# Optimization experiments

Hardware: AMD Instinct MI355X
Metric: run time of the kernel (lower is better)

Reference implementation:

```python
import jax, jax.numpy as jnp
import numpy as np

BATCH = 1024
INPUT_DIM = 4096
HIDDEN_DIM = 4096
N_BLOCKS = 8
BLOCK_SIZE = HIDDEN_DIM // N_BLOCKS          # 512
IN_BLOCK_SIZE = INPUT_DIM // N_BLOCKS        # 512


def setup_inputs() -> dict:
    key = jax.random.key(0)
    ks = jax.random.split(key, 6)
    scale = 1.0 / np.sqrt(BLOCK_SIZE)  # torch GRUCell init: U(-1/sqrt(hidden), 1/sqrt(hidden))
    return {
        "x": jax.random.normal(ks[0], (BATCH, INPUT_DIM), dtype=jnp.float32),
        "h": jax.random.normal(ks[1], (BATCH, HIDDEN_DIM), dtype=jnp.float32),
        "W_ih": jax.random.normal(ks[2], (N_BLOCKS, 3 * BLOCK_SIZE, IN_BLOCK_SIZE), dtype=jnp.float32) * scale,
        "W_hh": jax.random.normal(ks[3], (N_BLOCKS, 3 * BLOCK_SIZE, BLOCK_SIZE), dtype=jnp.float32) * scale,
        "b_ih": jax.random.normal(ks[4], (N_BLOCKS, 3 * BLOCK_SIZE), dtype=jnp.float32) * scale,
        "b_hh": jax.random.normal(ks[5], (N_BLOCKS, 3 * BLOCK_SIZE), dtype=jnp.float32) * scale,
    }


def reference(x, h, W_ih, W_hh, b_ih, b_hh):
    B = x.shape[0]
    n, g3, ibs = W_ih.shape           # n_blocks, 3*block_size, input_block_size
    bs = W_hh.shape[2]                # block_size
    xb = x.reshape(B, n, ibs)         # (B, n_blocks, input_block_size)
    hb = h.reshape(B, n, bs)          # (B, n_blocks, block_size)
    # Block-diagonal GEMM: one grouped matmul over all blocks at once.
    gi = jnp.einsum('bni,ngi->bng', xb, W_ih) + b_ih   # (B, n, 3*bs)
    gh = jnp.einsum('bnh,ngh->bng', hb, W_hh) + b_hh   # (B, n, 3*bs)
    i_r, i_z, i_n = jnp.split(gi, 3, axis=-1)
    h_r, h_z, h_n = jnp.split(gh, 3, axis=-1)
    r = jax.nn.sigmoid(i_r + h_r)                      # reset gate
    z = jax.nn.sigmoid(i_z + h_z)                      # update gate
    n_gate = jnp.tanh(i_n + r * h_n)                   # candidate state
    new_h = n_gate + z * (hb - n_gate)                 # torch GRUCell: h' = (1-z)*n + z*h
    return new_h.reshape(B, n * bs)
```

## Files before the change

### kernel.cpp

```cpp
#include <hip/hip_runtime.h>
#include <hip/hip_bf16.h>
#include <stdint.h>

#define G1CAST(p) ((const __attribute__((address_space(1))) void*)(p))
#define L3CAST(p) ((__attribute__((address_space(3))) void*)(p))

typedef short bf16x8 __attribute__((ext_vector_type(8)));
typedef float f32x16 __attribute__((ext_vector_type(16)));

static __device__ __forceinline__ short f2bf(float f) {
    __hip_bfloat16 b = __float2bfloat16(f);
    return __builtin_bit_cast(short, b);
}

__global__ __launch_bounds__(256) void wconv_kernel(const float* __restrict__ Wih,
                                                    const float* __restrict__ Whh,
                                                    short* __restrict__ Wcat) {
    const int tid = blockIdx.x * 256 + threadIdx.x;
    const int64_t e = (int64_t)tid * 8;
    const int kk = (int)(e & 1023);
    const int row = (int)(e >> 10);
    const int n = row / 1536;
    const int gr = row - n * 1536;
    const float* src = (kk < 512)
        ? Wih + ((int64_t)n * 786432 + (int64_t)gr * 512 + kk)
        : Whh + ((int64_t)n * 786432 + (int64_t)gr * 512 + (kk - 512));
    const float4 a = ((const float4*)src)[0];
    const float4 b = ((const float4*)src)[1];
    bf16x8 o;
    o[0] = f2bf(a.x); o[1] = f2bf(a.y); o[2] = f2bf(a.z); o[3] = f2bf(a.w);
    o[4] = f2bf(b.x); o[5] = f2bf(b.y); o[6] = f2bf(b.z); o[7] = f2bf(b.w);
    *(bf16x8*)(Wcat + e) = o;
}

__global__ __launch_bounds__(256) void aconv_kernel(const float* __restrict__ x,
                                                    const float* __restrict__ h,
                                                    short* __restrict__ Aimg) {
    const int gid = blockIdx.x * 256 + threadIdx.x;
    const int q = gid & 511;
    const int tile = gid >> 9;
    const int c4 = q & 3;
    const int r = q >> 2;
    const int ks = tile & 31;
    const int nblk = (tile >> 5) & 7;
    const int bt = tile >> 8;
    const float* base = (ks < 16) ? x : h;
    const float* src = base + ((size_t)(bt * 128 + r) * 4096
                               + nblk * 512 + (ks & 15) * 32 + c4 * 8);
    const float4 a = ((const float4*)src)[0];
    const float4 b = ((const float4*)src)[1];
    bf16x8 o;
    o[0] = f2bf(a.x); o[1] = f2bf(a.y); o[2] = f2bf(a.z); o[3] = f2bf(a.w);
    o[4] = f2bf(b.x); o[5] = f2bf(b.y); o[6] = f2bf(b.z); o[7] = f2bf(b.w);
    *(bf16x8*)(Aimg + (size_t)tile * 4096 + r * 32 + ((c4 ^ ((r >> 1) & 3)) * 8)) = o;
}

__global__ __launch_bounds__(512, 4) void gru_kernel(
    const float* __restrict__ hst,
    const short* __restrict__ Wcat, const short* __restrict__ Aimg,
    const float* __restrict__ b_ih, const float* __restrict__ b_hh,
    float* __restrict__ out)
{
    __shared__ short ldsA[4][128 * 32];
    __shared__ short ldsB[4][3 * 64 * 32];

    const int tid = threadIdx.x;
    const int nblk = blockIdx.x & 7;
    const int rr_ = blockIdx.x >> 3;
    const int bt = rr_ >> 3;
    const int jt = rr_ & 7;
    const int j0b = jt * 64;
    const int brow0 = bt * 128;

    const int lane = tid & 63;
    const int wave = tid >> 6;
    const int wm = wave >> 1;
    const int wn = wave & 1;
    const int l31 = lane & 31;
    const int k8 = lane >> 5;

    const int bj  = (tid & 255) >> 2;
    const int cir = tid & 3;
    const int g1  = tid >> 8;
    const size_t bsrc1 = ((size_t)nblk * 1536 + (size_t)g1 * 512 + (size_t)(j0b + bj)) * 1024
                       + (size_t)((cir ^ ((bj >> 1) & 3)) * 8);
    const size_t bsrc2 = bsrc1 + (size_t)2 * 512 * 1024;
    const size_t a_tile0 = ((size_t)(bt * 8 + nblk) * 32) << 13;

    f32x16 acc_r = {};
    f32x16 acc_z = {};
    f32x16 acc_nx = {};
    f32x16 acc_nh = {};

    auto stage = [&](int buf, int ks) {
        const char* asrc = (const char*)Aimg + a_tile0 + ((size_t)ks << 13) + (size_t)tid * 16;
        __builtin_amdgcn_global_load_lds(G1CAST(asrc),
                                         L3CAST((char*)&ldsA[buf][0] + tid * 16), 16, 0, 0);
        const short* ws = Wcat + (size_t)ks * 32;
        __builtin_amdgcn_global_load_lds(G1CAST(ws + bsrc1),
                                         L3CAST((char*)&ldsB[buf][0] + tid * 16), 16, 0, 0);
        if (tid < 256)
            __builtin_amdgcn_global_load_lds(G1CAST(ws + bsrc2),
                                             L3CAST((char*)&ldsB[buf][0] + 8192 + tid * 16), 16, 0, 0);
    };

    const int arow = wm * 32 + l31;
    const int aoff = arow * 64;
    const int aswz = ((arow >> 1) & 3) << 4;
    const int jl = wn * 32 + l31;
    const int boff = jl * 64;
    const int bswz = ((jl >> 1) & 3) << 4;

    auto computeStep = [&](const short* Ab_s, const short* Bb_s, f32x16& accN) {
        const char* Ab = (const char*)Ab_s;
        const char* Bb = (const char*)Bb_s;
        #pragma unroll
        for (int ksub = 0; ksub < 2; ++ksub) {
            const int kb = ksub * 32 + k8 * 16;
            bf16x8 af = *(const bf16x8*)(Ab + aoff + (kb ^ aswz));
            bf16x8 b0 = *(const bf16x8*)(Bb + 0 * 4096 + boff + (kb ^ bswz));
            bf16x8 b1 = *(const bf16x8*)(Bb + 1 * 4096 + boff + (kb ^ bswz));
            bf16x8 b2 = *(const bf16x8*)(Bb + 2 * 4096 + boff + (kb ^ bswz));
            acc_r = __builtin_amdgcn_mfma_f32_32x32x16_bf16(af, b0, acc_r, 0, 0, 0);
            acc_z = __builtin_amdgcn_mfma_f32_32x32x16_bf16(af, b1, acc_z, 0, 0, 0);
            accN  = __builtin_amdgcn_mfma_f32_32x32x16_bf16(af, b2, accN, 0, 0, 0);
        }
    };

    stage(0, 0); stage(1, 1); stage(2, 2);

    #pragma unroll 1
    for (int i = 0; i < 16; ++i) {
        asm volatile("s_waitcnt vmcnt(4)" ::: "memory");
        __builtin_amdgcn_s_barrier();
        stage((i + 3) & 3, i + 3);
        computeStep(ldsA[i & 3], ldsB[i & 3], acc_nx);
    }
    #pragma unroll 1
    for (int i = 16; i < 29; ++i) {
        asm volatile("s_waitcnt vmcnt(4)" ::: "memory");
        __builtin_amdgcn_s_barrier();
        stage((i + 3) & 3, i + 3);
        computeStep(ldsA[i & 3], ldsB[i & 3], acc_nh);
    }
    asm volatile("s_waitcnt vmcnt(4)" ::: "memory");
    __builtin_amdgcn_s_barrier();
    computeStep(ldsA[29 & 3], ldsB[29 & 3], acc_nh);
    asm volatile("s_waitcnt vmcnt(2)" ::: "memory");
    __builtin_amdgcn_s_barrier();
    computeStep(ldsA[30 & 3], ldsB[30 & 3], acc_nh);
    asm volatile("s_waitcnt vmcnt(0)" ::: "memory");
    __builtin_amdgcn_s_barrier();
    computeStep(ldsA[31 & 3], ldsB[31 & 3], acc_nh);

    const int jb = j0b + wn * 32 + l31;
    const int bb = nblk * 1536 + jb;
    const float br = b_ih[bb] + b_hh[bb];
    const float bz = b_ih[bb + 512] + b_hh[bb + 512];
    const float bnx = b_ih[bb + 1024];
    const float bnh = b_hh[bb + 1024];
    const int gcol = nblk * 512 + jb;
    #pragma unroll
    for (int rr = 0; rr < 16; ++rr) {
        const int rowl = (rr & 3) + 8 * (rr >> 2) + 4 * k8;
        const int row = brow0 + wm * 32 + rowl;
        const size_t idx = (size_t)row * 4096 + gcol;
        const float sr = acc_r[rr] + br;
        const float sz = acc_z[rr] + bz;
        const float rg = 1.f / (1.f + __expf(-sr));
        const float zg = 1.f / (1.f + __expf(-sz));
        const float tin = (acc_nx[rr] + bnx) + rg * (acc_nh[rr] + bnh);
        const float e2 = __expf(-2.f * tin);
        const float ng = 2.f / (1.f + e2) - 1.f;
        const float hv = hst[idx];
        out[idx] = ng + zg * (hv - ng);
    }
}

extern "C" void kernel_launch(void* const* d_in, const int* in_sizes, int n_in,
                              void* d_out, int out_size, void* d_ws, size_t ws_size,
                              hipStream_t stream) {
    (void)in_sizes; (void)n_in; (void)out_size; (void)ws_size;
    const float* x    = (const float*)d_in[0];
    const float* h    = (const float*)d_in[1];
    const float* W_ih = (const float*)d_in[2];
    const float* W_hh = (const float*)d_in[3];
    const float* b_ih = (const float*)d_in[4];
    const float* b_hh = (const float*)d_in[5];
    short* Wcat = (short*)d_ws;
    short* Aimg = (short*)d_ws + (size_t)12 * 1024 * 1024;

    wconv_kernel<<<6144, 256, 0, stream>>>(W_ih, W_hh, Wcat);
    aconv_kernel<<<4096, 256, 0, stream>>>(x, h, Aimg);
    gru_kernel<<<512, 512, 0, stream>>>(h, Wcat, Aimg, b_ih, b_hh, (float*)d_out);
}
```

Before: 61.02 us.

## Double batch tile to 256 rows so each block reuses weights across two M sub-tiles

Each workgroup now covers 256 batch rows instead of 128, with each wave computing two 32-row MFMA sub-tiles that share the same B fragments. The A-image layout and staging loads change to match, the grid halves to 256 blocks, and launch bounds drop to 2 blocks per CU. This halves weight traffic per output but doubles accumulator registers and leaves only one block per CU, which reduces latency hiding.

```diff
diff --git a/kernel.cpp b/kernel.cpp
--- a/kernel.cpp
+++ b/kernel.cpp
@@ -37,32 +37,31 @@
                                                     const float* __restrict__ h,
                                                     short* __restrict__ Aimg) {
     const int gid = blockIdx.x * 256 + threadIdx.x;
-    const int q = gid & 511;
-    const int tile = gid >> 9;
-    const int c4 = q & 3;
-    const int r = q >> 2;
+    const int c4 = gid & 3;
+    const int r = (gid >> 2) & 255;
+    const int tile = gid >> 10;
     const int ks = tile & 31;
     const int nblk = (tile >> 5) & 7;
     const int bt = tile >> 8;
     const float* base = (ks < 16) ? x : h;
-    const float* src = base + ((size_t)(bt * 128 + r) * 4096
+    const float* src = base + ((size_t)(bt * 256 + r) * 4096
                                + nblk * 512 + (ks & 15) * 32 + c4 * 8);
     const float4 a = ((const float4*)src)[0];
     const float4 b = ((const float4*)src)[1];
     bf16x8 o;
     o[0] = f2bf(a.x); o[1] = f2bf(a.y); o[2] = f2bf(a.z); o[3] = f2bf(a.w);
     o[4] = f2bf(b.x); o[5] = f2bf(b.y); o[6] = f2bf(b.z); o[7] = f2bf(b.w);
-    *(bf16x8*)(Aimg + (size_t)tile * 4096 + r * 32 + ((c4 ^ ((r >> 1) & 3)) * 8)) = o;
-}
-
-__global__ __launch_bounds__(512, 4) void gru_kernel(
+    *(bf16x8*)(Aimg + (size_t)tile * 8192 + r * 32 + ((c4 ^ ((r >> 1) & 3)) * 8)) = o;
+}
+
+__global__ __launch_bounds__(512, 2) void gru_kernel(
     const float* __restrict__ hst,
     const short* __restrict__ Wcat, const short* __restrict__ Aimg,
     const float* __restrict__ b_ih, const float* __restrict__ b_hh,
     float* __restrict__ out)
 {
-    __shared__ short ldsA[4][128 * 32];
-    __shared__ short ldsB[4][3 * 64 * 32];
+    __shared__ short ldsA[4][8192];
+    __shared__ short ldsB[4][8192];
 
     const int tid = threadIdx.x;
     const int nblk = blockIdx.x & 7;
@@ -70,7 +69,7 @@
     const int bt = rr_ >> 3;
     const int jt = rr_ & 7;
     const int j0b = jt * 64;
-    const int brow0 = bt * 128;
+    const int brow0 = bt * 256;
 
     const int lane = tid & 63;
     const int wave = tid >> 6;
@@ -79,51 +78,58 @@
     const int l31 = lane & 31;
     const int k8 = lane >> 5;
 
-    const int bj  = (tid & 255) >> 2;
-    const int cir = tid & 3;
-    const int g1  = tid >> 8;
-    const size_t bsrc1 = ((size_t)nblk * 1536 + (size_t)g1 * 512 + (size_t)(j0b + bj)) * 1024
-                       + (size_t)((cir ^ ((bj >> 1) & 3)) * 8);
-    const size_t bsrc2 = bsrc1 + (size_t)2 * 512 * 1024;
-    const size_t a_tile0 = ((size_t)(bt * 8 + nblk) * 32) << 13;
-
-    f32x16 acc_r = {};
-    f32x16 acc_z = {};
-    f32x16 acc_nx = {};
-    f32x16 acc_nh = {};
+    auto bsrc_of = [&](int c) -> size_t {
+        const int g = c >> 8, j = (c & 255) >> 2, ci = c & 3;
+        return ((size_t)nblk * 1536 + (size_t)g * 512 + (size_t)(j0b + j)) * 1024
+             + (size_t)((ci ^ ((j >> 1) & 3)) * 8);
+    };
+    const size_t bsrc0 = bsrc_of(tid);
+    const size_t bsrc1 = bsrc_of(tid < 256 ? tid + 512 : tid + 256);
+    const size_t a_tile0 = ((size_t)(bt * 8 + nblk) * 32) << 14;
+
+    f32x16 acc_r[2] = {};
+    f32x16 acc_z[2] = {};
+    f32x16 acc_nx[2] = {};
+    f32x16 acc_nh[2] = {};
 
     auto stage = [&](int buf, int ks) {
-        const char* asrc = (const char*)Aimg + a_tile0 + ((size_t)ks << 13) + (size_t)tid * 16;
-        __builtin_amdgcn_global_load_lds(G1CAST(asrc),
-                                         L3CAST((char*)&ldsA[buf][0] + tid * 16), 16, 0, 0);
+        const char* asrc = (const char*)Aimg + a_tile0 + ((size_t)ks << 14) + (size_t)tid * 16;
+        char* adst = (char*)&ldsA[buf][0] + tid * 16;
+        __builtin_amdgcn_global_load_lds(G1CAST(asrc), L3CAST(adst), 16, 0, 0);
+        __builtin_amdgcn_global_load_lds(G1CAST(asrc + 8192), L3CAST(adst + 8192), 16, 0, 0);
         const short* ws = Wcat + (size_t)ks * 32;
-        __builtin_amdgcn_global_load_lds(G1CAST(ws + bsrc1),
-                                         L3CAST((char*)&ldsB[buf][0] + tid * 16), 16, 0, 0);
-        if (tid < 256)
-            __builtin_amdgcn_global_load_lds(G1CAST(ws + bsrc2),
-                                             L3CAST((char*)&ldsB[buf][0] + 8192 + tid * 16), 16, 0, 0);
+        char* bdst = (char*)&ldsB[buf][0] + tid * 16;
+        __builtin_amdgcn_global_load_lds(G1CAST(ws + bsrc0), L3CAST(bdst), 16, 0, 0);
+        __builtin_amdgcn_global_load_lds(G1CAST(ws + bsrc1), L3CAST(bdst + 8192), 16, 0, 0);
     };
 
-    const int arow = wm * 32 + l31;
-    const int aoff = arow * 64;
-    const int aswz = ((arow >> 1) & 3) << 4;
     const int jl = wn * 32 + l31;
     const int boff = jl * 64;
     const int bswz = ((jl >> 1) & 3) << 4;
-
-    auto computeStep = [&](const short* Ab_s, const short* Bb_s, f32x16& accN) {
+    const int arow0 = wm * 64 + l31;
+    const int arow1 = arow0 + 32;
+    const int aoff0 = arow0 * 64;
+    const int aoff1 = arow1 * 64;
+    const int aswz0 = ((arow0 >> 1) & 3) << 4;
+    const int aswz1 = ((arow1 >> 1) & 3) << 4;
+
+    auto computeStep = [&](const short* Ab_s, const short* Bb_s, f32x16 (&accN)[2]) {
         const char* Ab = (const char*)Ab_s;
         const char* Bb = (const char*)Bb_s;
         #pragma unroll
         for (int ksub = 0; ksub < 2; ++ksub) {
             const int kb = ksub * 32 + k8 * 16;
-            bf16x8 af = *(const bf16x8*)(Ab + aoff + (kb ^ aswz));
+            bf16x8 af0 = *(const bf16x8*)(Ab + aoff0 + (kb ^ aswz0));
+            bf16x8 af1 = *(const bf16x8*)(Ab + aoff1 + (kb ^ aswz1));
             bf16x8 b0 = *(const bf16x8*)(Bb + 0 * 4096 + boff + (kb ^ bswz));
             bf16x8 b1 = *(const bf16x8*)(Bb + 1 * 4096 + boff + (kb ^ bswz));
             bf16x8 b2 = *(const bf16x8*)(Bb + 2 * 4096 + boff + (kb ^ bswz));
-            acc_r = __builtin_amdgcn_mfma_f32_32x32x16_bf16(af, b0, acc_r, 0, 0, 0);
-            acc_z = __builtin_amdgcn_mfma_f32_32x32x16_bf16(af, b1, acc_z, 0, 0, 0);
-            accN  = __builtin_amdgcn_mfma_f32_32x32x16_bf16(af, b2, accN, 0, 0, 0);
+            acc_r[0] = __builtin_amdgcn_mfma_f32_32x32x16_bf16(af0, b0, acc_r[0], 0, 0, 0);
+            acc_r[1] = __builtin_amdgcn_mfma_f32_32x32x16_bf16(af1, b0, acc_r[1], 0, 0, 0);
+            acc_z[0] = __builtin_amdgcn_mfma_f32_32x32x16_bf16(af0, b1, acc_z[0], 0, 0, 0);
+            acc_z[1] = __builtin_amdgcn_mfma_f32_32x32x16_bf16(af1, b1, acc_z[1], 0, 0, 0);
+            accN[0]  = __builtin_amdgcn_mfma_f32_32x32x16_bf16(af0, b2, accN[0], 0, 0, 0);
+            accN[1]  = __builtin_amdgcn_mfma_f32_32x32x16_bf16(af1, b2, accN[1], 0, 0, 0);
         }
     };
 
@@ -131,25 +137,30 @@
 
     #pragma unroll 1
     for (int i = 0; i < 16; ++i) {
-        asm volatile("s_waitcnt vmcnt(4)" ::: "memory");
+        asm volatile("s_waitcnt vmcnt(8)" ::: "memory");
+        __builtin_amdgcn_sched_barrier(0);
         __builtin_amdgcn_s_barrier();
         stage((i + 3) & 3, i + 3);
         computeStep(ldsA[i & 3], ldsB[i & 3], acc_nx);
     }
     #pragma unroll 1
     for (int i = 16; i < 29; ++i) {
-        asm volatile("s_waitcnt vmcnt(4)" ::: "memory");
+        asm volatile("s_waitcnt vmcnt(8)" ::: "memory");
+        __builtin_amdgcn_sched_barrier(0);
         __builtin_amdgcn_s_barrier();
         stage((i + 3) & 3, i + 3);
         computeStep(ldsA[i & 3], ldsB[i & 3], acc_nh);
     }
-    asm volatile("s_waitcnt vmcnt(4)" ::: "memory");
+    asm volatile("s_waitcnt vmcnt(8)" ::: "memory");
+    __builtin_amdgcn_sched_barrier(0);
     __builtin_amdgcn_s_barrier();
     computeStep(ldsA[29 & 3], ldsB[29 & 3], acc_nh);
-    asm volatile("s_waitcnt vmcnt(2)" ::: "memory");
+    asm volatile("s_waitcnt vmcnt(4)" ::: "memory");
+    __builtin_amdgcn_sched_barrier(0);
     __builtin_amdgcn_s_barrier();
     computeStep(ldsA[30 & 3], ldsB[30 & 3], acc_nh);
     asm volatile("s_waitcnt vmcnt(0)" ::: "memory");
+    __builtin_amdgcn_sched_barrier(0);
     __builtin_amdgcn_s_barrier();
     computeStep(ldsA[31 & 3], ldsB[31 & 3], acc_nh);
 
@@ -161,19 +172,22 @@
     const float bnh = b_hh[bb + 1024];
     const int gcol = nblk * 512 + jb;
     #pragma unroll
-    for (int rr = 0; rr < 16; ++rr) {
-        const int rowl = (rr & 3) + 8 * (rr >> 2) + 4 * k8;
-        const int row = brow0 + wm * 32 + rowl;
-        const size_t idx = (size_t)row * 4096 + gcol;
-        const float sr = acc_r[rr] + br;
-        const float sz = acc_z[rr] + bz;
-        const float rg = 1.f / (1.f + __expf(-sr));
-        const float zg = 1.f / (1.f + __expf(-sz));
-        const float tin = (acc_nx[rr] + bnx) + rg * (acc_nh[rr] + bnh);
-        const float e2 = __expf(-2.f * tin);
-        const float ng = 2.f / (1.f + e2) - 1.f;
-        const float hv = hst[idx];
-        out[idx] = ng + zg * (hv - ng);
+    for (int m = 0; m < 2; ++m) {
+        #pragma unroll
+        for (int rr = 0; rr < 16; ++rr) {
+            const int rowl = (rr & 3) + 8 * (rr >> 2) + 4 * k8;
+            const int row = brow0 + wm * 64 + m * 32 + rowl;
+            const size_t idx = (size_t)row * 4096 + gcol;
+            const float sr = acc_r[m][rr] + br;
+            const float sz = acc_z[m][rr] + bz;
+            const float rg = 1.f / (1.f + __expf(-sr));
+            const float zg = 1.f / (1.f + __expf(-sz));
+            const float tin = (acc_nx[m][rr] + bnx) + rg * (acc_nh[m][rr] + bnh);
+            const float e2 = __expf(-2.f * tin);
+            const float ng = 2.f / (1.f + e2) - 1.f;
+            const float hv = hst[idx];
+            out[idx] = ng + zg * (hv - ng);
+        }
     }
 }
 
@@ -192,5 +206,5 @@
 
     wconv_kernel<<<6144, 256, 0, stream>>>(W_ih, W_hh, Wcat);
     aconv_kernel<<<4096, 256, 0, stream>>>(x, h, Aimg);
-    gru_kernel<<<512, 512, 0, stream>>>(h, Wcat, Aimg, b_ih, b_hh, (float*)d_out);
-}
+    gru_kernel<<<256, 512, 0, stream>>>(h, Wcat, Aimg, b_ih, b_hh, (float*)d_out);
+}
```

New measurement: 69.95 us. 14.6% more time.
